# Optimization experiments

Measured on AMD Instinct MI355X. Metric: run time of the kernel, lower is better.

The kernel has to match this reference:

```python
import jax, jax.numpy as jnp
import numpy as np

NUM_SUBJECTS = 2048
NUM_TRIALS = 40  # -> num_paths = C(43,3) = 12341
NUM_STATES = 4


def _enumerate_paths(num_trials):
    # All monotone non-decreasing state sequences over {0,1,2,3}, same order
    # as the torch cached_property `paths`.
    paths = [[0], [1], [2], [3]]
    for _ in range(num_trials - 1):
        paths = [p + [s] for p in paths for s in range(p[-1], NUM_STATES)]
    return np.asarray(paths, dtype=np.int32)  # [P, T]


def setup_inputs() -> dict:
    key = jax.random.key(0)
    k1, k2, k3, k4 = jax.random.split(key, 4)
    return {
        "subject_responses": jax.random.randint(
            k1, (NUM_SUBJECTS, NUM_TRIALS), 0, NUM_STATES, dtype=jnp.int32),
        "paths": jnp.asarray(_enumerate_paths(NUM_TRIALS)),
        "w_strategy_success": jax.random.uniform(k2, (4, 4), dtype=jnp.float32),
        "w_state_priors": jax.random.uniform(k3, (4,), dtype=jnp.float32),
        "w_transitions": jax.random.uniform(k4, (4, 4), dtype=jnp.float32),
    }


def reference(subject_responses, paths, w_strategy_success, w_state_priors,
              w_transitions):
    # Fixed constants from the module
    strat_mask = jnp.triu(jnp.full((4, 4), -jnp.inf, dtype=jnp.float32), k=1)
    trans_mask = jnp.tril(jnp.full((4, 4), -jnp.inf, dtype=jnp.float32), k=-1)
    p_strategy_responses = jnp.array(
        [[3 / 9, 4 / 9, 1 / 9, 1 / 9],
         [0.0, 4 / 6, 1 / 6, 1 / 6],
         [0.0, 0.0, 0.5, 0.5],
         [0.0, 0.0, 0.0, 1.0]], dtype=jnp.float32)

    # Parameter transforms
    p_strategy_success = jax.nn.softmax(w_strategy_success + strat_mask, axis=-1)
    p_state_responses = p_strategy_success @ p_strategy_responses        # [4,4]
    p_state_priors = jax.nn.softmax(w_state_priors)                      # [4]
    p_transitions = jax.nn.softmax(w_transitions + trans_mask, axis=-1)  # [4,4]

    # P(path): log prior of first state + sum of log transition probs
    log_tr = jnp.log(p_transitions)
    log_p_paths = (jnp.log(p_state_priors)[paths[:, 0]]
                   + log_tr[paths[:, :-1], paths[:, 1:]].sum(-1))  # [P]
    p_paths = jnp.exp(log_p_paths)

    # P(responses | path) per subject: sum_t log p_state_responses[state_t, resp_t]
    # expressed as a dense contraction (P, T*4) x (T*4, S) for efficiency.
    log_sr = jnp.log(p_state_responses)                  # [state, response]
    paths_oh = jax.nn.one_hot(paths, NUM_STATES, dtype=log_sr.dtype)  # [P,T,4]
    resp_log = log_sr.T[subject_responses]               # [S,T,4]; [s,t,k]=log_sr[k, r_st]
    log_lik = jnp.einsum('ptk,stk->sp', paths_oh, resp_log)  # [S,P]
    likelihoods = jnp.exp(log_lik)

    # P(path | responses)
    numerator = p_paths[None, :] * likelihoods           # [S,P]
    posteriors = numerator / numerator.sum(-1, keepdims=True)
    return posteriors
```

## Files before the change

### kernel.cpp

```cpp
#include <hip/hip_runtime.h>
#include <math.h>

#define NSUB   2048
#define NTRIAL 40
#define NPATH  12341
#define PBLK   1024
#define NFULL  (NPATH / PBLK)
#define NTAIL  (NPATH - NFULL * PBLK)

#define LOG2E  1.44269504088896340736f

__global__ __launch_bounds__(64) void path_kernel(
        const int* __restrict__ paths,
        const float* __restrict__ w_sp,
        const float* __restrict__ w_tr,
        int2* __restrict__ rec) {
    __shared__ float sprior[4];
    __shared__ float str[16];
    const int tid = threadIdx.x;

    if (tid < 4) {
        float m = fmaxf(fmaxf(w_sp[0], w_sp[1]), fmaxf(w_sp[2], w_sp[3]));
        float s = 0.f;
        for (int k = 0; k < 4; k++) s += __expf(w_sp[k] - m);
        sprior[tid] = (w_sp[tid] - (__logf(s) + m)) * LOG2E;
    } else if (tid < 20) {
        int idx = tid - 4, i = idx >> 2, j = idx & 3;
        float m = -1e30f;
        for (int k = i; k < 4; k++) m = fmaxf(m, w_tr[i*4 + k]);
        float s = 0.f;
        for (int k = i; k < 4; k++) s += __expf(w_tr[i*4 + k] - m);
        str[idx] = (j >= i) ? (w_tr[i*4 + j] - (__logf(s) + m)) * LOG2E : 0.f;
    }
    __syncthreads();

    int p = blockIdx.x * 64 + tid;
    if (p >= NPATH) return;

    const int4* pp = (const int4*)(paths + (size_t)p * NTRIAL);
    int st[NTRIAL];
#pragma unroll
    for (int q = 0; q < NTRIAL / 4; q++) {
        int4 v = pp[q];
        st[4*q] = v.x; st[4*q+1] = v.y; st[4*q+2] = v.z; st[4*q+3] = v.w;
    }
    float lp = sprior[st[0]];
    int c0 = (st[0] == 0), c1 = (st[0] <= 1), c2 = (st[0] <= 2);
#pragma unroll
    for (int t = 1; t < NTRIAL; t++) {
        lp += str[st[t-1]*4 + st[t]];
        c0 += (st[t] == 0); c1 += (st[t] <= 1); c2 += (st[t] <= 2);
    }
    rec[p] = make_int2(__float_as_int(lp), c0 | (c1 << 6) | (c2 << 12));
}

__global__ __launch_bounds__(1024) void post_kernel(
        const int* __restrict__ resp,
        const float* __restrict__ w_ss,
        const int2* __restrict__ rec,
        float* __restrict__ out) {
    __shared__ float lsr[16];
    __shared__ int   rs[NTRIAL];
    __shared__ float D1[NTRIAL + 1], D2[NTRIAL + 1], D3[NTRIAL + 1];
    __shared__ float red[16];
    __shared__ float s_inv;

    const int s = blockIdx.x;
    const int tid = threadIdx.x;
    const int lane = tid & 63, wave = tid >> 6;

    if (wave == 3 && lane < NTRIAL)
        rs[lane] = resp[(size_t)s * NTRIAL + lane];
    if (tid < 16) {
        const float psr[4][4] = {
            {3.f/9.f, 4.f/9.f, 1.f/9.f, 1.f/9.f},
            {0.f,     4.f/6.f, 1.f/6.f, 1.f/6.f},
            {0.f,     0.f,     0.5f,    0.5f},
            {0.f,     0.f,     0.f,     1.f}};
        int i = tid >> 2, r = tid & 3;
        float m = -1e30f;
        for (int j = 0; j <= i; j++) m = fmaxf(m, w_ss[i*4 + j]);
        float e[4] = {0.f,0.f,0.f,0.f}, ssum = 0.f;
        for (int j = 0; j <= i; j++) { e[j] = __expf(w_ss[i*4 + j] - m); ssum += e[j]; }
        float acc = 0.f;
        for (int j = 0; j <= i; j++) acc += (e[j] / ssum) * psr[j][r];
        lsr[tid] = __builtin_amdgcn_logf(acc);
    }
    __syncthreads();

    if (wave < 3) {
        float x = 0.f;
        if (lane < NTRIAL) {
            int rv = rs[lane];
            x = lsr[wave*4 + rv] - lsr[wave*4 + 4 + rv];
        }
#pragma unroll
        for (int off = 1; off < 64; off <<= 1) {
            float y = __shfl_up(x, off, 64);
            if (lane >= off) x += y;
        }
        float* D = (wave == 0) ? D1 : (wave == 1) ? D2 : D3;
        if (lane < NTRIAL) D[lane + 1] = x;
        if (lane == 0)     D[0] = 0.f;
    }
    __syncthreads();

    int2 r[NFULL];
#pragma unroll
    for (int i = 0; i < NFULL; i++) r[i] = rec[tid + PBLK * i];
    const bool tail = (tid < NTAIL);
    int2 rt = tail ? rec[NFULL * PBLK + tid] : make_int2(0, 0);

    float nums[NFULL];
    float lsum = 0.f;
#pragma unroll
    for (int i = 0; i < NFULL; i++) {
        int b = r[i].y;
        int t1 = b & 63, t2 = (b >> 6) & 63, t3 = (b >> 12) & 63;
        float v = __builtin_amdgcn_exp2f(
            __int_as_float(r[i].x) + D1[t1] + D2[t2] + D3[t3]);
        nums[i] = v;
        lsum += v;
    }
    float numt = 0.f;
    if (tail) {
        int b = rt.y;
        int t1 = b & 63, t2 = (b >> 6) & 63, t3 = (b >> 12) & 63;
        numt = __builtin_amdgcn_exp2f(
            __int_as_float(rt.x) + D1[t1] + D2[t2] + D3[t3]);
        lsum += numt;
    }

#pragma unroll
    for (int off = 32; off > 0; off >>= 1)
        lsum += __shfl_down(lsum, off, 64);
    if (lane == 0) red[wave] = lsum;
    __syncthreads();
    if (tid < 64) {
        float t = (lane < 16) ? red[lane] : 0.f;
#pragma unroll
        for (int off = 8; off > 0; off >>= 1)
            t += __shfl_down(t, off, 64);
        if (lane == 0) s_inv = 1.f / t;
    }
    __syncthreads();
    const float inv = s_inv;

    float* orow = out + (size_t)s * NPATH;
#pragma unroll
    for (int i = 0; i < NFULL; i++)
        __builtin_nontemporal_store(nums[i] * inv, &orow[tid + PBLK * i]);
    if (tail)
        __builtin_nontemporal_store(numt * inv, &orow[NFULL * PBLK + tid]);
}

extern "C" void kernel_launch(void* const* d_in, const int* in_sizes, int n_in,
                              void* d_out, int out_size, void* d_ws, size_t ws_size,
                              hipStream_t stream) {
    const int*   resp  = (const int*)d_in[0];
    const int*   paths = (const int*)d_in[1];
    const float* w_ss  = (const float*)d_in[2];
    const float* w_sp  = (const float*)d_in[3];
    const float* w_tr  = (const float*)d_in[4];
    float* out = (float*)d_out;

    int2* rec = (int2*)d_ws;

    path_kernel<<<(NPATH + 63) / 64, 64, 0, stream>>>(paths, w_sp, w_tr, rec);
    post_kernel<<<NSUB, PBLK, 0, stream>>>(resp, w_ss, rec, out);
}
```

Baseline: 136.9 us.

## Process eight subjects per block, reusing path records held in registers

The posterior kernel now handles eight subjects per 1024-thread block instead of one. The per-path records are loaded into registers once and reused across all eight subjects. The setup work (log response table, prefix sums over each subject's responses) is amortised by splitting it across waves for all eight subjects. A per-subject constant for the state-3 term is added to the exponent; it cancels in normalisation but improves numerical range. The grid shrinks to 256 blocks, which reduces parallelism and serialises the per-subject reductions and barriers inside each block.

```diff
diff --git a/kernel.cpp b/kernel.cpp
--- a/kernel.cpp
+++ b/kernel.cpp
@@ -7,6 +7,8 @@
 #define PBLK   1024
 #define NFULL  (NPATH / PBLK)
 #define NTAIL  (NPATH - NFULL * PBLK)
+#define SPB    8
+#define NBLK   (NSUB / SPB)
 
 #define LOG2E  1.44269504088896340736f
 
@@ -54,104 +56,126 @@
     rec[p] = make_int2(__float_as_int(lp), c0 | (c1 << 6) | (c2 << 12));
 }
 
-__global__ __launch_bounds__(1024) void post_kernel(
+__global__ __launch_bounds__(1024, 4) void post_kernel(
         const int* __restrict__ resp,
         const float* __restrict__ w_ss,
         const int2* __restrict__ rec,
         float* __restrict__ out) {
     __shared__ float lsr[16];
-    __shared__ int   rs[NTRIAL];
-    __shared__ float D1[NTRIAL + 1], D2[NTRIAL + 1], D3[NTRIAL + 1];
+    __shared__ int   rs[SPB * NTRIAL];
+    __shared__ float D[SPB][3][NTRIAL + 1];
     __shared__ float red[16];
     __shared__ float s_inv;
+    __shared__ float s_ct3[SPB];
 
-    const int s = blockIdx.x;
-    const int tid = threadIdx.x;
+    const int tid  = threadIdx.x;
     const int lane = tid & 63, wave = tid >> 6;
+    const int sbase = blockIdx.x * SPB;
 
-    if (wave == 3 && lane < NTRIAL)
-        rs[lane] = resp[(size_t)s * NTRIAL + lane];
-    if (tid < 16) {
+    float lp[NFULL]; int bp[NFULL];
+#pragma unroll
+    for (int i = 0; i < NFULL; i++) {
+        int2 rr = rec[tid + PBLK * i];
+        lp[i] = __int_as_float(rr.x); bp[i] = rr.y;
+    }
+    const bool tail = (tid < NTAIL);
+    float lpt = 0.f; int bpt = 0;
+    if (tail) {
+        int2 rr = rec[NFULL * PBLK + tid];
+        lpt = __int_as_float(rr.x); bpt = rr.y;
+    }
+
+    if (tid < SPB * NTRIAL)
+        rs[tid] = resp[(size_t)sbase * NTRIAL + tid];
+    if (wave == 15 && lane < 16) {
         const float psr[4][4] = {
             {3.f/9.f, 4.f/9.f, 1.f/9.f, 1.f/9.f},
             {0.f,     4.f/6.f, 1.f/6.f, 1.f/6.f},
             {0.f,     0.f,     0.5f,    0.5f},
             {0.f,     0.f,     0.f,     1.f}};
-        int i = tid >> 2, r = tid & 3;
+        int i = lane >> 2, rr = lane & 3;
         float m = -1e30f;
         for (int j = 0; j <= i; j++) m = fmaxf(m, w_ss[i*4 + j]);
         float e[4] = {0.f,0.f,0.f,0.f}, ssum = 0.f;
         for (int j = 0; j <= i; j++) { e[j] = __expf(w_ss[i*4 + j] - m); ssum += e[j]; }
         float acc = 0.f;
-        for (int j = 0; j <= i; j++) acc += (e[j] / ssum) * psr[j][r];
-        lsr[tid] = __builtin_amdgcn_logf(acc);
+        for (int j = 0; j <= i; j++) acc += (e[j] / ssum) * psr[j][rr];
+        lsr[lane] = __builtin_amdgcn_logf(acc);
     }
     __syncthreads();
 
-    if (wave < 3) {
-        float x = 0.f;
-        if (lane < NTRIAL) {
-            int rv = rs[lane];
-            x = lsr[wave*4 + rv] - lsr[wave*4 + 4 + rv];
+#pragma unroll
+    for (int task = wave; task < 4 * SPB; task += 16) {
+        const int su = task >> 2, role = task & 3;
+        if (role < 3) {
+            float x = 0.f;
+            if (lane < NTRIAL) {
+                int rv = rs[su * NTRIAL + lane];
+                x = lsr[role*4 + rv] - lsr[role*4 + 4 + rv];
+            }
+#pragma unroll
+            for (int off = 1; off < 64; off <<= 1) {
+                float y = __shfl_up(x, off, 64);
+                if (lane >= off) x += y;
+            }
+            if (lane < NTRIAL) D[su][role][lane + 1] = x;
+            if (lane == 0)     D[su][role][0] = 0.f;
+        } else {
+            float t = (lane < NTRIAL) ? lsr[12 + rs[su * NTRIAL + lane]] : 0.f;
+#pragma unroll
+            for (int off = 32; off > 0; off >>= 1)
+                t += __shfl_down(t, off, 64);
+            if (lane == 0) s_ct3[su] = t;
         }
-#pragma unroll
-        for (int off = 1; off < 64; off <<= 1) {
-            float y = __shfl_up(x, off, 64);
-            if (lane >= off) x += y;
-        }
-        float* D = (wave == 0) ? D1 : (wave == 1) ? D2 : D3;
-        if (lane < NTRIAL) D[lane + 1] = x;
-        if (lane == 0)     D[0] = 0.f;
     }
     __syncthreads();
 
-    int2 r[NFULL];
+    for (int su = 0; su < SPB; su++) {
+        const float ct3 = s_ct3[su];
+        const float* __restrict__ D1 = D[su][0];
+        const float* __restrict__ D2 = D[su][1];
+        const float* __restrict__ D3 = D[su][2];
+
+        float nums[NFULL];
+        float lsum = 0.f;
 #pragma unroll
-    for (int i = 0; i < NFULL; i++) r[i] = rec[tid + PBLK * i];
-    const bool tail = (tid < NTAIL);
-    int2 rt = tail ? rec[NFULL * PBLK + tid] : make_int2(0, 0);
-
-    float nums[NFULL];
-    float lsum = 0.f;
-#pragma unroll
-    for (int i = 0; i < NFULL; i++) {
-        int b = r[i].y;
-        int t1 = b & 63, t2 = (b >> 6) & 63, t3 = (b >> 12) & 63;
-        float v = __builtin_amdgcn_exp2f(
-            __int_as_float(r[i].x) + D1[t1] + D2[t2] + D3[t3]);
-        nums[i] = v;
-        lsum += v;
-    }
-    float numt = 0.f;
-    if (tail) {
-        int b = rt.y;
-        int t1 = b & 63, t2 = (b >> 6) & 63, t3 = (b >> 12) & 63;
-        numt = __builtin_amdgcn_exp2f(
-            __int_as_float(rt.x) + D1[t1] + D2[t2] + D3[t3]);
-        lsum += numt;
-    }
+        for (int i = 0; i < NFULL; i++) {
+            int b = bp[i];
+            float v = __builtin_amdgcn_exp2f(
+                lp[i] + ct3 + D1[b & 63] + D2[(b >> 6) & 63] + D3[(b >> 12) & 63]);
+            nums[i] = v;
+            lsum += v;
+        }
+        float numt = 0.f;
+        if (tail) {
+            int b = bpt;
+            numt = __builtin_amdgcn_exp2f(
+                lpt + ct3 + D1[b & 63] + D2[(b >> 6) & 63] + D3[(b >> 12) & 63]);
+            lsum += numt;
+        }
 
 #pragma unroll
-    for (int off = 32; off > 0; off >>= 1)
-        lsum += __shfl_down(lsum, off, 64);
-    if (lane == 0) red[wave] = lsum;
-    __syncthreads();
-    if (tid < 64) {
-        float t = (lane < 16) ? red[lane] : 0.f;
+        for (int off = 32; off > 0; off >>= 1)
+            lsum += __shfl_down(lsum, off, 64);
+        if (lane == 0) red[wave] = lsum;
+        __syncthreads();
+        if (tid < 64) {
+            float t = (lane < 16) ? red[lane] : 0.f;
 #pragma unroll
-        for (int off = 8; off > 0; off >>= 1)
-            t += __shfl_down(t, off, 64);
-        if (lane == 0) s_inv = 1.f / t;
+            for (int off = 8; off > 0; off >>= 1)
+                t += __shfl_down(t, off, 64);
+            if (lane == 0) s_inv = 1.f / t;
+        }
+        __syncthreads();
+        const float inv = s_inv;
+
+        float* orow = out + (size_t)(sbase + su) * NPATH;
+#pragma unroll
+        for (int i = 0; i < NFULL; i++)
+            __builtin_nontemporal_store(nums[i] * inv, &orow[tid + PBLK * i]);
+        if (tail)
+            __builtin_nontemporal_store(numt * inv, &orow[NFULL * PBLK + tid]);
     }
-    __syncthreads();
-    const float inv = s_inv;
-
-    float* orow = out + (size_t)s * NPATH;
-#pragma unroll
-    for (int i = 0; i < NFULL; i++)
-        __builtin_nontemporal_store(nums[i] * inv, &orow[tid + PBLK * i]);
-    if (tail)
-        __builtin_nontemporal_store(numt * inv, &orow[NFULL * PBLK + tid]);
 }
 
 extern "C" void kernel_launch(void* const* d_in, const int* in_sizes, int n_in,
@@ -167,5 +191,5 @@
     int2* rec = (int2*)d_ws;
 
     path_kernel<<<(NPATH + 63) / 64, 64, 0, stream>>>(paths, w_sp, w_tr, rec);
-    post_kernel<<<NSUB, PBLK, 0, stream>>>(resp, w_ss, rec, out);
+    post_kernel<<<NBLK, PBLK, 0, stream>>>(resp, w_ss, rec, out);
 }
```

New measurement: 142.3 us. +4.0%, slower.
